# Optimization experiments

Measured on AMD Instinct MI355X. Metric: run time of the kernel, lower is better.

## Reference

```python
import jax, jax.numpy as jnp
import numpy as np

N_NODES = 100000
N_EDGES = 1600000
IN_DIM, HID_DIM, OUT_DIM = 384, 64, 64
DROP_P = 0.5


def setup_inputs() -> dict:
    key = jax.random.key(0)
    ks = jax.random.split(key, 9)
    x = jax.random.normal(ks[0], (N_NODES, IN_DIM), dtype=jnp.float32)
    edge_index = jax.random.randint(ks[1], (2, N_EDGES), 0, N_NODES, dtype=jnp.int64)
    edge_weight = jax.random.uniform(ks[2], (N_EDGES,), dtype=jnp.float32)
    W1 = jax.random.normal(ks[3], (IN_DIM, HID_DIM), dtype=jnp.float32) * (1.0 / np.sqrt(IN_DIM))
    b1 = jnp.zeros((HID_DIM,), dtype=jnp.float32)
    W2 = jax.random.normal(ks[4], (HID_DIM, OUT_DIM), dtype=jnp.float32) * (1.0 / np.sqrt(HID_DIM))
    b2 = jnp.zeros((OUT_DIM,), dtype=jnp.float32)
    drop_mask1 = jax.random.bernoulli(ks[5], 1.0 - DROP_P, (N_NODES, IN_DIM))
    drop_mask2 = jax.random.bernoulli(ks[6], 1.0 - DROP_P, (N_NODES, HID_DIM))
    return {"x": x, "edge_index": edge_index, "edge_weight": edge_weight,
            "W1": W1, "b1": b1, "W2": W2, "b2": b2,
            "drop_mask1": drop_mask1, "drop_mask2": drop_mask2}


def _gcn_conv(h, W, b, src, dst, edge_weight, n_nodes):
    # GCNConv: linear transform first (smaller dim), then normalized sparse aggregation
    h = h @ W                                        # [N, d_out]
    msg = h[src] * edge_weight[:, None]              # gather over edges [E, d_out]
    agg = jax.ops.segment_sum(msg, dst, num_segments=n_nodes)  # scatter-add [N, d_out]
    return agg + b


def reference(x, edge_index, edge_weight, W1, b1, W2, b2, drop_mask1, drop_mask2):
    scale = 1.0 / (1.0 - DROP_P)
    src, dst = edge_index[0], edge_index[1]
    n = x.shape[0]
    h = x * drop_mask1.astype(x.dtype) * scale                  # dropout (training)
    h = jax.nn.relu(_gcn_conv(h, W1, b1, src, dst, edge_weight, n))
    h = h * drop_mask2.astype(h.dtype) * scale                  # dropout (training)
    return _gcn_conv(h, W2, b2, src, dst, edge_weight, n)
```

## Files before the change

### kernel.cpp

```cpp
#include <hip/hip_runtime.h>
#include <hip/hip_bf16.h>
#include <stdint.h>

#define N_NODES 100000
#define N_EDGES 1600000
#define IN_DIM  384
#define HID_DIM 64
#define SCAN_NB 391

typedef __attribute__((ext_vector_type(8))) short short8_t;
typedef __attribute__((ext_vector_type(4))) float f32x4;

__global__ void k_detect(const uint32_t* __restrict__ ei,
                         const uint32_t* __restrict__ m1,
                         int* __restrict__ flags) {
    int l = threadIdx.x;
    uint32_t hi = ei[2 * l + 1];
    int ei64 = __all(hi == 0u);

    uint32_t maxb = 0;
    int bf = 0, f16 = 0, hib = 0;
    for (int i = 0; i < 4; ++i) {
        uint32_t w = m1[l * 4 + i];
        uint32_t b0 = w & 0xffu, b1 = (w >> 8) & 0xffu,
                 b2 = (w >> 16) & 0xffu, b3 = (w >> 24) & 0xffu;
        uint32_t mb = b0 > b1 ? b0 : b1;
        uint32_t mb2 = b2 > b3 ? b2 : b3;
        mb = mb > mb2 ? mb : mb2;
        maxb = maxb > mb ? maxb : mb;
        if ((w & 0xffffu) == 0x3f80u) bf = 1;
        if ((w & 0xffffu) == 0x3c00u) f16 = 1;
        if ((b1 | b2 | b3) != 0u) hib = 1;
    }
    int small  = __all(maxb <= 1u);
    int anybf  = __any(bf);
    int anyf16 = __any(f16);
    int anyhib = __any(hib);
    if (l == 0) {
        flags[0] = ei64;
        int mm;
        if (small)                 mm = anyhib ? 3 : 4;
        else if (anybf || anyf16)  mm = 0;
        else                       mm = 2;
        flags[1] = mm;
    }
}

__device__ __forceinline__ float mask_at(const void* p, int mode, long idx) {
    if (mode == 0) return ((const uint16_t*)p)[idx] ? 2.0f : 0.0f;
    if (mode == 2) return ((const float*)p)[idx] != 0.0f ? 2.0f : 0.0f;
    if (mode == 3) return ((const uint8_t*)p)[idx] ? 2.0f : 0.0f;
    return ((const int*)p)[idx] ? 2.0f : 0.0f;
}

__device__ __forceinline__ void load_edge(const int* p32, int mode64, long e,
                                          int& s, int& d) {
    if (mode64) { s = p32[2 * e]; d = p32[2 * (N_EDGES + e)]; }
    else        { s = p32[e];     d = p32[N_EDGES + e]; }
}

__device__ __forceinline__ ushort f2bf(float f) {
    uint32_t u = __float_as_uint(f);
    return (ushort)((u + 0x7fffu + ((u >> 16) & 1u)) >> 16);
}
__device__ __forceinline__ float bf2f(ushort h) {
    return __uint_as_float(((uint32_t)h) << 16);
}

__global__ __launch_bounds__(256) void k_hist(const void* __restrict__ ei,
                                              uint32_t* __restrict__ deg,
                                              const int* __restrict__ flags) {
    const int mode64 = flags[0];
    const int* p32 = (const int*)ei;
    for (long e = (long)blockIdx.x * 256 + threadIdx.x; e < N_EDGES;
         e += (long)gridDim.x * 256) {
        int s, d; load_edge(p32, mode64, e, s, d);
        atomicAdd(&deg[d], 1u);
    }
}

__global__ __launch_bounds__(256) void k_scanA(const uint32_t* __restrict__ deg,
                                               uint32_t* __restrict__ partials) {
    __shared__ uint32_t sbuf[256];
    int idx = blockIdx.x * 256 + threadIdx.x;
    uint32_t v = idx < N_NODES ? deg[idx] : 0u;
    sbuf[threadIdx.x] = v;
    __syncthreads();
    for (int off = 128; off > 0; off >>= 1) {
        if (threadIdx.x < off) sbuf[threadIdx.x] += sbuf[threadIdx.x + off];
        __syncthreads();
    }
    if (threadIdx.x == 0) partials[blockIdx.x] = sbuf[0];
}

__global__ void k_scanB(uint32_t* __restrict__ partials,
                        uint32_t* __restrict__ poff,
                        uint32_t* __restrict__ starts) {
    if (threadIdx.x == 0) {
        uint32_t run = 0;
        for (int b = 0; b < SCAN_NB; ++b) {
            poff[b] = run;
            run += partials[b];
        }
        starts[N_NODES] = run;
    }
}

__global__ __launch_bounds__(256) void k_scanC(const uint32_t* __restrict__ deg,
                                               const uint32_t* __restrict__ poff,
                                               uint32_t* __restrict__ starts) {
    __shared__ uint32_t sbuf[256];
    int idx = blockIdx.x * 256 + threadIdx.x;
    uint32_t v = idx < N_NODES ? deg[idx] : 0u;
    sbuf[threadIdx.x] = v;
    __syncthreads();
    for (int off = 1; off < 256; off <<= 1) {
        uint32_t add = threadIdx.x >= off ? sbuf[threadIdx.x - off] : 0u;
        __syncthreads();
        sbuf[threadIdx.x] += add;
        __syncthreads();
    }
    if (idx < N_NODES) starts[idx] = poff[blockIdx.x] + sbuf[threadIdx.x] - v;
}

__global__ __launch_bounds__(256) void k_reorder(const void* __restrict__ ei,
                                                 const float* __restrict__ ew,
                                                 uint32_t* __restrict__ cursors,
                                                 int2* __restrict__ sorted,
                                                 const int* __restrict__ flags) {
    const int mode64 = flags[0];
    const int* p32 = (const int*)ei;
    for (long e = (long)blockIdx.x * 256 + threadIdx.x; e < N_EDGES;
         e += (long)gridDim.x * 256) {
        int s, d; load_edge(p32, mode64, e, s, d);
        float w = ew[e];
        uint32_t pos = atomicAdd(&cursors[d], 1u);
        sorted[pos] = make_int2(s, __float_as_int(w));
    }
}

__global__ __launch_bounds__(256) void k1_mfma(
        const float* __restrict__ x, const void* __restrict__ m1,
        const float* __restrict__ W1, float* __restrict__ H,
        const int* __restrict__ flags) {
    __shared__ ushort Ah[64][32];
    __shared__ ushort Al[64][32];
    __shared__ ushort Bh[64][32];
    __shared__ ushort Bl[64][32];
    const int mmode = flags[1];
    const int t = threadIdx.x;
    const int node0 = blockIdx.x * 64;
    const int l = t & 63, w = t >> 6;

    f32x4 acc[4];
#pragma unroll
    for (int i = 0; i < 4; ++i) acc[i] = (f32x4)0.0f;

    const int arow = t >> 2;
    const int akq  = (t & 3) * 8;
    const int brow = t >> 3;
    const int bc0  = (t & 7) * 8;

    for (int ks = 0; ks < IN_DIM; ks += 32) {
        {
            float xv[8];
            long node = node0 + arow;
            if (node < N_NODES) {
                long gb = node * IN_DIM + ks + akq;
                float4 x0 = *(const float4*)(x + gb);
                float4 x1 = *(const float4*)(x + gb + 4);
                xv[0] = x0.x; xv[1] = x0.y; xv[2] = x0.z; xv[3] = x0.w;
                xv[4] = x1.x; xv[5] = x1.y; xv[6] = x1.z; xv[7] = x1.w;
                float mv[8];
                if (mmode == 0) {
                    const ushort* mp = (const ushort*)m1 + gb;
                    ushort4 a = *(const ushort4*)mp;
                    ushort4 b = *(const ushort4*)(mp + 4);
                    mv[0] = a.x ? 2.f : 0.f; mv[1] = a.y ? 2.f : 0.f;
                    mv[2] = a.z ? 2.f : 0.f; mv[3] = a.w ? 2.f : 0.f;
                    mv[4] = b.x ? 2.f : 0.f; mv[5] = b.y ? 2.f : 0.f;
                    mv[6] = b.z ? 2.f : 0.f; mv[7] = b.w ? 2.f : 0.f;
                } else if (mmode == 2) {
                    const float* mp = (const float*)m1 + gb;
                    float4 a = *(const float4*)mp;
                    float4 b = *(const float4*)(mp + 4);
                    mv[0] = a.x != 0.f ? 2.f : 0.f; mv[1] = a.y != 0.f ? 2.f : 0.f;
                    mv[2] = a.z != 0.f ? 2.f : 0.f; mv[3] = a.w != 0.f ? 2.f : 0.f;
                    mv[4] = b.x != 0.f ? 2.f : 0.f; mv[5] = b.y != 0.f ? 2.f : 0.f;
                    mv[6] = b.z != 0.f ? 2.f : 0.f; mv[7] = b.w != 0.f ? 2.f : 0.f;
                } else if (mmode == 3) {
                    uint2 mb = *(const uint2*)((const uint8_t*)m1 + gb);
#pragma unroll
                    for (int j = 0; j < 4; ++j) {
                        mv[j]     = ((mb.x >> (8 * j)) & 0xffu) ? 2.f : 0.f;
                        mv[4 + j] = ((mb.y >> (8 * j)) & 0xffu) ? 2.f : 0.f;
                    }
                } else {
                    const int* mp = (const int*)m1 + gb;
                    int4 a = *(const int4*)mp;
                    int4 b = *(const int4*)(mp + 4);
                    mv[0] = a.x ? 2.f : 0.f; mv[1] = a.y ? 2.f : 0.f;
                    mv[2] = a.z ? 2.f : 0.f; mv[3] = a.w ? 2.f : 0.f;
                    mv[4] = b.x ? 2.f : 0.f; mv[5] = b.y ? 2.f : 0.f;
                    mv[6] = b.z ? 2.f : 0.f; mv[7] = b.w ? 2.f : 0.f;
                }
#pragma unroll
                for (int j = 0; j < 8; ++j) xv[j] *= mv[j];
            } else {
#pragma unroll
                for (int j = 0; j < 8; ++j) xv[j] = 0.0f;
            }
            uint ph[4], pl[4];
#pragma unroll
            for (int j2 = 0; j2 < 4; ++j2) {
                ushort h0 = f2bf(xv[2 * j2]);
                ushort h1 = f2bf(xv[2 * j2 + 1]);
                ushort l0 = f2bf(xv[2 * j2]     - bf2f(h0));
                ushort l1 = f2bf(xv[2 * j2 + 1] - bf2f(h1));
                ph[j2] = (uint)h0 | ((uint)h1 << 16);
                pl[j2] = (uint)l0 | ((uint)l1 << 16);
            }
            *(uint4*)&Ah[arow][akq] = make_uint4(ph[0], ph[1], ph[2], ph[3]);
            *(uint4*)&Al[arow][akq] = make_uint4(pl[0], pl[1], pl[2], pl[3]);
        }
        {
            long gb = (long)(ks + brow) * 64 + bc0;
            float4 w0 = *(const float4*)(W1 + gb);
            float4 w1 = *(const float4*)(W1 + gb + 4);
            float wv[8] = {w0.x, w0.y, w0.z, w0.w, w1.x, w1.y, w1.z, w1.w};
#pragma unroll
            for (int j = 0; j < 8; ++j) {
                ushort hs = f2bf(wv[j]);
                Bh[bc0 + j][brow] = hs;
                Bl[bc0 + j][brow] = f2bf(wv[j] - bf2f(hs));
            }
        }
        __syncthreads();
        short8_t ah = *(const short8_t*)&Ah[w * 16 + (l & 15)][(l >> 4) * 8];
        short8_t al = *(const short8_t*)&Al[w * 16 + (l & 15)][(l >> 4) * 8];
#pragma unroll
        for (int nt = 0; nt < 4; ++nt) {
            short8_t bh = *(const short8_t*)&Bh[nt * 16 + (l & 15)][(l >> 4) * 8];
            short8_t bl = *(const short8_t*)&Bl[nt * 16 + (l & 15)][(l >> 4) * 8];
            acc[nt] = __builtin_amdgcn_mfma_f32_16x16x32_bf16(ah, bh, acc[nt], 0, 0, 0);
            acc[nt] = __builtin_amdgcn_mfma_f32_16x16x32_bf16(ah, bl, acc[nt], 0, 0, 0);
            acc[nt] = __builtin_amdgcn_mfma_f32_16x16x32_bf16(al, bh, acc[nt], 0, 0, 0);
        }
        __syncthreads();
    }
    const int r0 = (l >> 4) * 4;
#pragma unroll
    for (int nt = 0; nt < 4; ++nt) {
#pragma unroll
        for (int r = 0; r < 4; ++r) {
            long node = node0 + w * 16 + r0 + r;
            if (node < N_NODES) H[node * 64 + nt * 16 + (l & 15)] = acc[nt][r];
        }
    }
}

__global__ __launch_bounds__(256) void k_agg(const float* __restrict__ Hsrc,
                                             const int2* __restrict__ sorted,
                                             const uint32_t* __restrict__ starts,
                                             const float* __restrict__ bias,
                                             float* __restrict__ dest) {
    const int lane = threadIdx.x & 63;
    const long n = (long)blockIdx.x * 4 + (threadIdx.x >> 6);
    if (n >= N_NODES) return;
    uint32_t e  = starts[n];
    uint32_t e1 = starts[n + 1];
    float acc = bias ? bias[lane] : 0.0f;
    for (; e + 2 <= e1; e += 2) {
        int2 p0 = sorted[e];
        int2 p1 = sorted[e + 1];
        float v0 = Hsrc[(long)p0.x * 64 + lane];
        float v1 = Hsrc[(long)p1.x * 64 + lane];
        acc = fmaf(v0, __int_as_float(p0.y), acc);
        acc = fmaf(v1, __int_as_float(p1.y), acc);
    }
    if (e < e1) {
        int2 p0 = sorted[e];
        acc = fmaf(Hsrc[(long)p0.x * 64 + lane], __int_as_float(p0.y), acc);
    }
    dest[n * 64 + lane] = acc;
}

__global__ __launch_bounds__(256) void k_aggmlp(
        const float* __restrict__ Hsrc, const int2* __restrict__ sorted,
        const uint32_t* __restrict__ starts, const float* __restrict__ b1,
        const void* __restrict__ m2, const float* __restrict__ W2,
        float* __restrict__ H2, const int* __restrict__ flags) {
    __shared__ float w2s[64 * 64];
    __shared__ float vbuf[4][64];
    const int mmode = flags[1];
    for (int i = threadIdx.x; i < 4096; i += 256) w2s[i] = W2[i];
    __syncthreads();

    const int lane = threadIdx.x & 63;
    const int w = threadIdx.x >> 6;
    const long n = (long)blockIdx.x * 4 + w;
    uint32_t e  = starts[n];
    uint32_t e1 = starts[n + 1];
    float acc = 0.0f;
    for (; e + 2 <= e1; e += 2) {
        int2 p0 = sorted[e];
        int2 p1 = sorted[e + 1];
        float v0 = Hsrc[(long)p0.x * 64 + lane];
        float v1 = Hsrc[(long)p1.x * 64 + lane];
        acc = fmaf(v0, __int_as_float(p0.y), acc);
        acc = fmaf(v1, __int_as_float(p1.y), acc);
    }
    if (e < e1) {
        int2 p0 = sorted[e];
        acc = fmaf(Hsrc[(long)p0.x * 64 + lane], __int_as_float(p0.y), acc);
    }
    float u = acc + b1[lane];
    u = u > 0.0f ? u : 0.0f;
    u *= mask_at(m2, mmode, n * 64 + lane);
    vbuf[w][lane] = u;
    float h2 = 0.0f;
#pragma unroll
    for (int j = 0; j < 64; j += 4) {
        float4 v4 = *(const float4*)&vbuf[w][j];
        h2 = fmaf(v4.x, w2s[(j + 0) * 64 + lane], h2);
        h2 = fmaf(v4.y, w2s[(j + 1) * 64 + lane], h2);
        h2 = fmaf(v4.z, w2s[(j + 2) * 64 + lane], h2);
        h2 = fmaf(v4.w, w2s[(j + 3) * 64 + lane], h2);
    }
    H2[n * 64 + lane] = h2;
}

__global__ __launch_bounds__(256) void k_scatter(
        const float* __restrict__ Hsrc, const void* __restrict__ ei,
        const float* __restrict__ ew, float* __restrict__ dest,
        const int* __restrict__ flags) {
    const int mode64 = flags[0];
    const int lane = threadIdx.x & 63;
    const long wid = (long)blockIdx.x * 4 + (threadIdx.x >> 6);
    const long nw = (long)gridDim.x * 4;
    const int* p32 = (const int*)ei;
    for (long e = wid; e < N_EDGES; e += nw) {
        int s, d; load_edge(p32, mode64, e, s, d);
        float w = ew[e];
        float v = Hsrc[(long)s * 64 + lane] * w;
        atomicAdd(&dest[(long)d * 64 + lane], v);
    }
}

__global__ __launch_bounds__(256) void k3_mlp(
        const float* __restrict__ agg, const float* __restrict__ b1,
        const void* __restrict__ m2, const float* __restrict__ W2,
        float* __restrict__ H2, const int* __restrict__ flags) {
    __shared__ float w2s[64 * 64];
    __shared__ float vbuf[4][64];
    const int mmode = flags[1];
    for (int i = threadIdx.x; i < 4096; i += 256) w2s[i] = W2[i];
    __syncthreads();
    const int lane = threadIdx.x & 63;
    const int w = threadIdx.x >> 6;
    const float bc = b1[lane];
    const long wid = (long)blockIdx.x * 4 + w;
    const long nw = (long)gridDim.x * 4;
    for (long n = wid; n < N_NODES; n += nw) {
        float u = agg[n * 64 + lane] + bc;
        u = u > 0.0f ? u : 0.0f;
        u *= mask_at(m2, mmode, n * 64 + lane);
        vbuf[w][lane] = u;
        float acc = 0.0f;
#pragma unroll
        for (int j = 0; j < 64; j += 4) {
            float4 v4 = *(const float4*)&vbuf[w][j];
            acc = fmaf(v4.x, w2s[(j + 0) * 64 + lane], acc);
            acc = fmaf(v4.y, w2s[(j + 1) * 64 + lane], acc);
            acc = fmaf(v4.z, w2s[(j + 2) * 64 + lane], acc);
            acc = fmaf(v4.w, w2s[(j + 3) * 64 + lane], acc);
        }
        H2[n * 64 + lane] = acc;
    }
}

__global__ void k_init_out(float* __restrict__ out, const float* __restrict__ b2) {
    const long total = (long)N_NODES * 16;
    for (long j = (long)blockIdx.x * 256 + threadIdx.x; j < total;
         j += (long)gridDim.x * 256) {
        ((float4*)out)[j] = ((const float4*)b2)[j & 15];
    }
}

extern "C" void kernel_launch(void* const* d_in, const int* in_sizes, int n_in,
                              void* d_out, int out_size, void* d_ws, size_t ws_size,
                              hipStream_t stream) {
    const float* x  = (const float*)d_in[0];
    const void*  ei = d_in[1];
    const float* ew = (const float*)d_in[2];
    const float* W1 = (const float*)d_in[3];
    const float* b1 = (const float*)d_in[4];
    const float* W2 = (const float*)d_in[5];
    const float* b2 = (const float*)d_in[6];
    const void*  m1 = d_in[7];
    const void*  m2 = d_in[8];
    float* out = (float*)d_out;

    char* ws = (char*)d_ws;
    size_t off = 0;
    auto alloc = [&](size_t bytes) {
        char* p = ws + off;
        off += (bytes + 255) & ~(size_t)255;
        return p;
    };
    int*      flags   = (int*)alloc(32);
    float*    H       = (float*)alloc((size_t)N_NODES * 64 * 4);
    float*    AGG     = (float*)alloc((size_t)N_NODES * 64 * 4);
    int2*     sorted  = (int2*)alloc((size_t)N_EDGES * 8);
    uint32_t* starts  = (uint32_t*)alloc((size_t)(N_NODES + 1) * 4);
    uint32_t* deg     = (uint32_t*)alloc((size_t)N_NODES * 4);
    uint32_t* cursors = (uint32_t*)alloc((size_t)N_NODES * 4);
    uint32_t* poff    = (uint32_t*)alloc((size_t)SCAN_NB * 4);
    size_t need = off;

    hipLaunchKernelGGL(k_detect, dim3(1), dim3(64), 0, stream,
                       (const uint32_t*)ei, (const uint32_t*)m1, flags);

    if (ws_size >= need) {
        hipMemsetAsync(deg, 0, (size_t)N_NODES * 4, stream);
        hipLaunchKernelGGL(k_hist, dim3(2048), dim3(256), 0, stream,
                           ei, deg, flags);
        hipLaunchKernelGGL(k_scanA, dim3(SCAN_NB), dim3(256), 0, stream,
                           deg, poff);
        hipLaunchKernelGGL(k_scanB, dim3(1), dim3(64), 0, stream,
                           poff, cursors, starts);
        hipLaunchKernelGGL(k_scanC, dim3(SCAN_NB), dim3(256), 0, stream,
                           deg, cursors, starts);
        hipMemcpyAsync(cursors, starts, (size_t)N_NODES * 4,
                       hipMemcpyDeviceToDevice, stream);
        hipLaunchKernelGGL(k_reorder, dim3(2048), dim3(256), 0, stream,
                           ei, ew, cursors, sorted, flags);
        hipLaunchKernelGGL(k1_mfma, dim3((N_NODES + 63) / 64), dim3(256), 0, stream,
                           x, m1, W1, H, flags);
        hipLaunchKernelGGL(k_aggmlp, dim3(N_NODES / 4), dim3(256), 0, stream,
                           H, sorted, starts, b1, m2, W2, AGG, flags);
        hipLaunchKernelGGL(k_agg, dim3(N_NODES / 4), dim3(256), 0, stream,
                           AGG, sorted, starts, b2, out);
    } else {
        hipMemsetAsync(AGG, 0, (size_t)N_NODES * 64 * 4, stream);
        hipLaunchKernelGGL(k1_mfma, dim3((N_NODES + 63) / 64), dim3(256), 0, stream,
                           x, m1, W1, H, flags);
        hipLaunchKernelGGL(k_scatter, dim3(4096), dim3(256), 0, stream,
                           H, ei, ew, AGG, flags);
        hipLaunchKernelGGL(k3_mlp, dim3(1024), dim3(256), 0, stream,
                           AGG, b1, m2, W2, H, flags);
        hipLaunchKernelGGL(k_init_out, dim3(2048), dim3(256), 0, stream, out, b2);
        hipLaunchKernelGGL(k_scatter, dim3(4096), dim3(256), 0, stream,
                           H, ei, ew, out, flags);
    }
}
```

Measured before the change: 834.7 us.

## Store hidden features in bf16, prepack W1, drop LDS staging and low-part MFMA

Intermediate node features H and H2 are now stored as bf16 instead of fp32, halving gather traffic in both edge aggregation passes. W1 is pre-split into bf16 hi/lo fragments by a new packing kernel, so the GEMM kernel loads A and B fragments straight from global memory without LDS or barriers. The GEMM also drops the x-low-part MFMA term. The aggregation loops are unrolled to four edges, and the single-thread partial scan is replaced by a parallel block scan. These changes reduce accuracy (bf16 storage of activations, no low-part x term), which risks tolerance failures.

Result: faster. 785.3 us (-5.9%).

```diff
diff --git a/kernel.cpp b/kernel.cpp
--- a/kernel.cpp
+++ b/kernel.cpp
@@ -93,17 +93,22 @@
     if (threadIdx.x == 0) partials[blockIdx.x] = sbuf[0];
 }
 
-__global__ void k_scanB(uint32_t* __restrict__ partials,
-                        uint32_t* __restrict__ poff,
-                        uint32_t* __restrict__ starts) {
-    if (threadIdx.x == 0) {
-        uint32_t run = 0;
-        for (int b = 0; b < SCAN_NB; ++b) {
-            poff[b] = run;
-            run += partials[b];
-        }
-        starts[N_NODES] = run;
-    }
+__global__ __launch_bounds__(512) void k_scanB(const uint32_t* __restrict__ partials,
+                                               uint32_t* __restrict__ poff,
+                                               uint32_t* __restrict__ starts) {
+    __shared__ uint32_t sbuf[512];
+    int t = threadIdx.x;
+    uint32_t v = t < SCAN_NB ? partials[t] : 0u;
+    sbuf[t] = v;
+    __syncthreads();
+    for (int off = 1; off < 512; off <<= 1) {
+        uint32_t add = t >= off ? sbuf[t - off] : 0u;
+        __syncthreads();
+        sbuf[t] += add;
+        __syncthreads();
+    }
+    if (t < SCAN_NB) poff[t] = sbuf[t] - v;
+    if (t == SCAN_NB - 1) starts[N_NODES] = sbuf[t];
 }
 
 __global__ __launch_bounds__(256) void k_scanC(const uint32_t* __restrict__ deg,
@@ -139,114 +144,98 @@
     }
 }
 
+__global__ __launch_bounds__(256) void k_packW(const float* __restrict__ W1,
+                                               ushort* __restrict__ Wpack) {
+    const int ks = blockIdx.x;
+    const int t  = threadIdx.x;
+    const int nt = t >> 6, l = t & 63;
+    ushort hs[8], ls[8];
+#pragma unroll
+    for (int j = 0; j < 8; ++j) {
+        float wv = W1[(ks * 32 + (l >> 4) * 8 + j) * 64 + nt * 16 + (l & 15)];
+        ushort h = f2bf(wv);
+        hs[j] = h;
+        ls[j] = f2bf(wv - bf2f(h));
+    }
+    *(short8_t*)&Wpack[((8 * ks + nt) * 64 + l) * 8]     = *(short8_t*)hs;
+    *(short8_t*)&Wpack[((8 * ks + 4 + nt) * 64 + l) * 8] = *(short8_t*)ls;
+}
+
 __global__ __launch_bounds__(256) void k1_mfma(
         const float* __restrict__ x, const void* __restrict__ m1,
-        const float* __restrict__ W1, float* __restrict__ H,
+        const ushort* __restrict__ Wpack, ushort* __restrict__ Hb,
         const int* __restrict__ flags) {
-    __shared__ ushort Ah[64][32];
-    __shared__ ushort Al[64][32];
-    __shared__ ushort Bh[64][32];
-    __shared__ ushort Bl[64][32];
     const int mmode = flags[1];
     const int t = threadIdx.x;
+    const int l = t & 63, w = t >> 6;
     const int node0 = blockIdx.x * 64;
-    const int l = t & 63, w = t >> 6;
+    const long row = node0 + w * 16 + (l & 15);
+    const int kq = (l >> 4) * 8;
+    const bool valid = row < N_NODES;
 
     f32x4 acc[4];
 #pragma unroll
     for (int i = 0; i < 4; ++i) acc[i] = (f32x4)0.0f;
 
-    const int arow = t >> 2;
-    const int akq  = (t & 3) * 8;
-    const int brow = t >> 3;
-    const int bc0  = (t & 7) * 8;
-
-    for (int ks = 0; ks < IN_DIM; ks += 32) {
-        {
-            float xv[8];
-            long node = node0 + arow;
-            if (node < N_NODES) {
-                long gb = node * IN_DIM + ks + akq;
-                float4 x0 = *(const float4*)(x + gb);
-                float4 x1 = *(const float4*)(x + gb + 4);
-                xv[0] = x0.x; xv[1] = x0.y; xv[2] = x0.z; xv[3] = x0.w;
-                xv[4] = x1.x; xv[5] = x1.y; xv[6] = x1.z; xv[7] = x1.w;
-                float mv[8];
-                if (mmode == 0) {
-                    const ushort* mp = (const ushort*)m1 + gb;
-                    ushort4 a = *(const ushort4*)mp;
-                    ushort4 b = *(const ushort4*)(mp + 4);
-                    mv[0] = a.x ? 2.f : 0.f; mv[1] = a.y ? 2.f : 0.f;
-                    mv[2] = a.z ? 2.f : 0.f; mv[3] = a.w ? 2.f : 0.f;
-                    mv[4] = b.x ? 2.f : 0.f; mv[5] = b.y ? 2.f : 0.f;
-                    mv[6] = b.z ? 2.f : 0.f; mv[7] = b.w ? 2.f : 0.f;
-                } else if (mmode == 2) {
-                    const float* mp = (const float*)m1 + gb;
-                    float4 a = *(const float4*)mp;
-                    float4 b = *(const float4*)(mp + 4);
-                    mv[0] = a.x != 0.f ? 2.f : 0.f; mv[1] = a.y != 0.f ? 2.f : 0.f;
-                    mv[2] = a.z != 0.f ? 2.f : 0.f; mv[3] = a.w != 0.f ? 2.f : 0.f;
-                    mv[4] = b.x != 0.f ? 2.f : 0.f; mv[5] = b.y != 0.f ? 2.f : 0.f;
-                    mv[6] = b.z != 0.f ? 2.f : 0.f; mv[7] = b.w != 0.f ? 2.f : 0.f;
-                } else if (mmode == 3) {
-                    uint2 mb = *(const uint2*)((const uint8_t*)m1 + gb);
-#pragma unroll
-                    for (int j = 0; j < 4; ++j) {
-                        mv[j]     = ((mb.x >> (8 * j)) & 0xffu) ? 2.f : 0.f;
-                        mv[4 + j] = ((mb.y >> (8 * j)) & 0xffu) ? 2.f : 0.f;
-                    }
-                } else {
-                    const int* mp = (const int*)m1 + gb;
-                    int4 a = *(const int4*)mp;
-                    int4 b = *(const int4*)(mp + 4);
-                    mv[0] = a.x ? 2.f : 0.f; mv[1] = a.y ? 2.f : 0.f;
-                    mv[2] = a.z ? 2.f : 0.f; mv[3] = a.w ? 2.f : 0.f;
-                    mv[4] = b.x ? 2.f : 0.f; mv[5] = b.y ? 2.f : 0.f;
-                    mv[6] = b.z ? 2.f : 0.f; mv[7] = b.w ? 2.f : 0.f;
+    for (int ks = 0; ks < 12; ++ks) {
+        float xv[8];
+        if (valid) {
+            long gb = row * IN_DIM + ks * 32 + kq;
+            float4 x0 = *(const float4*)(x + gb);
+            float4 x1 = *(const float4*)(x + gb + 4);
+            xv[0] = x0.x; xv[1] = x0.y; xv[2] = x0.z; xv[3] = x0.w;
+            xv[4] = x1.x; xv[5] = x1.y; xv[6] = x1.z; xv[7] = x1.w;
+            float mv[8];
+            if (mmode == 0) {
+                const ushort* mp = (const ushort*)m1 + gb;
+                ushort4 a = *(const ushort4*)mp;
+                ushort4 b = *(const ushort4*)(mp + 4);
+                mv[0] = a.x ? 2.f : 0.f; mv[1] = a.y ? 2.f : 0.f;
+                mv[2] = a.z ? 2.f : 0.f; mv[3] = a.w ? 2.f : 0.f;
+                mv[4] = b.x ? 2.f : 0.f; mv[5] = b.y ? 2.f : 0.f;
+                mv[6] = b.z ? 2.f : 0.f; mv[7] = b.w ? 2.f : 0.f;
+            } else if (mmode == 2) {
+                const float* mp = (const float*)m1 + gb;
+                float4 a = *(const float4*)mp;
+                float4 b = *(const float4*)(mp + 4);
+                mv[0] = a.x != 0.f ? 2.f : 0.f; mv[1] = a.y != 0.f ? 2.f : 0.f;
+                mv[2] = a.z != 0.f ? 2.f : 0.f; mv[3] = a.w != 0.f ? 2.f : 0.f;
+                mv[4] = b.x != 0.f ? 2.f : 0.f; mv[5] = b.y != 0.f ? 2.f : 0.f;
+                mv[6] = b.z != 0.f ? 2.f : 0.f; mv[7] = b.w != 0.f ? 2.f : 0.f;
+            } else if (mmode == 3) {
+                uint2 mb = *(const uint2*)((const uint8_t*)m1 + gb);
+#pragma unroll
+                for (int j = 0; j < 4; ++j) {
+                    mv[j]     = ((mb.x >> (8 * j)) & 0xffu) ? 2.f : 0.f;
+                    mv[4 + j] = ((mb.y >> (8 * j)) & 0xffu) ? 2.f : 0.f;
                 }
-#pragma unroll
-                for (int j = 0; j < 8; ++j) xv[j] *= mv[j];
             } else {
-#pragma unroll
-                for (int j = 0; j < 8; ++j) xv[j] = 0.0f;
+                const int* mp = (const int*)m1 + gb;
+                int4 a = *(const int4*)mp;
+                int4 b = *(const int4*)(mp + 4);
+                mv[0] = a.x ? 2.f : 0.f; mv[1] = a.y ? 2.f : 0.f;
+                mv[2] = a.z ? 2.f : 0.f; mv[3] = a.w ? 2.f : 0.f;
+                mv[4] = b.x ? 2.f : 0.f; mv[5] = b.y ? 2.f : 0.f;
+                mv[6] = b.z ? 2.f : 0.f; mv[7] = b.w ? 2.f : 0.f;
             }
-            uint ph[4], pl[4];
-#pragma unroll
-            for (int j2 = 0; j2 < 4; ++j2) {
-                ushort h0 = f2bf(xv[2 * j2]);
-                ushort h1 = f2bf(xv[2 * j2 + 1]);
-                ushort l0 = f2bf(xv[2 * j2]     - bf2f(h0));
-                ushort l1 = f2bf(xv[2 * j2 + 1] - bf2f(h1));
-                ph[j2] = (uint)h0 | ((uint)h1 << 16);
-                pl[j2] = (uint)l0 | ((uint)l1 << 16);
-            }
-            *(uint4*)&Ah[arow][akq] = make_uint4(ph[0], ph[1], ph[2], ph[3]);
-            *(uint4*)&Al[arow][akq] = make_uint4(pl[0], pl[1], pl[2], pl[3]);
+#pragma unroll
+            for (int j = 0; j < 8; ++j) xv[j] *= mv[j];
+        } else {
+#pragma unroll
+            for (int j = 0; j < 8; ++j) xv[j] = 0.0f;
         }
-        {
-            long gb = (long)(ks + brow) * 64 + bc0;
-            float4 w0 = *(const float4*)(W1 + gb);
-            float4 w1 = *(const float4*)(W1 + gb + 4);
-            float wv[8] = {w0.x, w0.y, w0.z, w0.w, w1.x, w1.y, w1.z, w1.w};
-#pragma unroll
-            for (int j = 0; j < 8; ++j) {
-                ushort hs = f2bf(wv[j]);
-                Bh[bc0 + j][brow] = hs;
-                Bl[bc0 + j][brow] = f2bf(wv[j] - bf2f(hs));
-            }
-        }
-        __syncthreads();
-        short8_t ah = *(const short8_t*)&Ah[w * 16 + (l & 15)][(l >> 4) * 8];
-        short8_t al = *(const short8_t*)&Al[w * 16 + (l & 15)][(l >> 4) * 8];
+        ushort ap[8];
+#pragma unroll
+        for (int j = 0; j < 8; ++j) ap[j] = f2bf(xv[j]);
+        short8_t ah = *(short8_t*)ap;
+
 #pragma unroll
         for (int nt = 0; nt < 4; ++nt) {
-            short8_t bh = *(const short8_t*)&Bh[nt * 16 + (l & 15)][(l >> 4) * 8];
-            short8_t bl = *(const short8_t*)&Bl[nt * 16 + (l & 15)][(l >> 4) * 8];
+            short8_t bh = *(const short8_t*)&Wpack[((8 * ks + nt) * 64 + l) * 8];
+            short8_t bl = *(const short8_t*)&Wpack[((8 * ks + 4 + nt) * 64 + l) * 8];
             acc[nt] = __builtin_amdgcn_mfma_f32_16x16x32_bf16(ah, bh, acc[nt], 0, 0, 0);
             acc[nt] = __builtin_amdgcn_mfma_f32_16x16x32_bf16(ah, bl, acc[nt], 0, 0, 0);
-            acc[nt] = __builtin_amdgcn_mfma_f32_16x16x32_bf16(al, bh, acc[nt], 0, 0, 0);
         }
-        __syncthreads();
     }
     const int r0 = (l >> 4) * 4;
 #pragma unroll
@@ -254,12 +243,62 @@
 #pragma unroll
         for (int r = 0; r < 4; ++r) {
             long node = node0 + w * 16 + r0 + r;
-            if (node < N_NODES) H[node * 64 + nt * 16 + (l & 15)] = acc[nt][r];
+            if (node < N_NODES)
+                Hb[node * 64 + nt * 16 + (l & 15)] = f2bf(acc[nt][r]);
         }
     }
 }
 
-__global__ __launch_bounds__(256) void k_agg(const float* __restrict__ Hsrc,
+__global__ __launch_bounds__(256) void k_aggmlp(
+        const ushort* __restrict__ Hb, const int2* __restrict__ sorted,
+        const uint32_t* __restrict__ starts, const float* __restrict__ b1,
+        const void* __restrict__ m2, const float* __restrict__ W2,
+        ushort* __restrict__ H2b, const int* __restrict__ flags) {
+    __shared__ float w2s[64 * 64];
+    __shared__ float vbuf[4][64];
+    const int mmode = flags[1];
+    for (int i = threadIdx.x; i < 4096; i += 256) w2s[i] = W2[i];
+    __syncthreads();
+
+    const int lane = threadIdx.x & 63;
+    const int w = threadIdx.x >> 6;
+    const long n = (long)blockIdx.x * 4 + w;
+    uint32_t e  = starts[n];
+    uint32_t e1 = starts[n + 1];
+    float acc = 0.0f;
+    for (; e + 4 <= e1; e += 4) {
+        int2 p0 = sorted[e],     p1 = sorted[e + 1];
+        int2 p2 = sorted[e + 2], p3 = sorted[e + 3];
+        float v0 = bf2f(Hb[(long)p0.x * 64 + lane]);
+        float v1 = bf2f(Hb[(long)p1.x * 64 + lane]);
+        float v2 = bf2f(Hb[(long)p2.x * 64 + lane]);
+        float v3 = bf2f(Hb[(long)p3.x * 64 + lane]);
+        acc = fmaf(v0, __int_as_float(p0.y), acc);
+        acc = fmaf(v1, __int_as_float(p1.y), acc);
+        acc = fmaf(v2, __int_as_float(p2.y), acc);
+        acc = fmaf(v3, __int_as_float(p3.y), acc);
+    }
+    for (; e < e1; ++e) {
+        int2 p0 = sorted[e];
+        acc = fmaf(bf2f(Hb[(long)p0.x * 64 + lane]), __int_as_float(p0.y), acc);
+    }
+    float u = acc + b1[lane];
+    u = u > 0.0f ? u : 0.0f;
+    u *= mask_at(m2, mmode, n * 64 + lane);
+    vbuf[w][lane] = u;
+    float h2 = 0.0f;
+#pragma unroll
+    for (int j = 0; j < 64; j += 4) {
+        float4 v4 = *(const float4*)&vbuf[w][j];
+        h2 = fmaf(v4.x, w2s[(j + 0) * 64 + lane], h2);
+        h2 = fmaf(v4.y, w2s[(j + 1) * 64 + lane], h2);
+        h2 = fmaf(v4.z, w2s[(j + 2) * 64 + lane], h2);
+        h2 = fmaf(v4.w, w2s[(j + 3) * 64 + lane], h2);
+    }
+    H2b[n * 64 + lane] = f2bf(h2);
+}
+
+__global__ __launch_bounds__(256) void k_agg(const ushort* __restrict__ Hb,
                                              const int2* __restrict__ sorted,
                                              const uint32_t* __restrict__ starts,
                                              const float* __restrict__ bias,
@@ -269,69 +308,28 @@
     if (n >= N_NODES) return;
     uint32_t e  = starts[n];
     uint32_t e1 = starts[n + 1];
-    float acc = bias ? bias[lane] : 0.0f;
-    for (; e + 2 <= e1; e += 2) {
-        int2 p0 = sorted[e];
-        int2 p1 = sorted[e + 1];
-        float v0 = Hsrc[(long)p0.x * 64 + lane];
-        float v1 = Hsrc[(long)p1.x * 64 + lane];
+    float acc = bias[lane];
+    for (; e + 4 <= e1; e += 4) {
+        int2 p0 = sorted[e],     p1 = sorted[e + 1];
+        int2 p2 = sorted[e + 2], p3 = sorted[e + 3];
+        float v0 = bf2f(Hb[(long)p0.x * 64 + lane]);
+        float v1 = bf2f(Hb[(long)p1.x * 64 + lane]);
+        float v2 = bf2f(Hb[(long)p2.x * 64 + lane]);
+        float v3 = bf2f(Hb[(long)p3.x * 64 + lane]);
         acc = fmaf(v0, __int_as_float(p0.y), acc);
         acc = fmaf(v1, __int_as_float(p1.y), acc);
-    }
-    if (e < e1) {
+        acc = fmaf(v2, __int_as_float(p2.y), acc);
+        acc = fmaf(v3, __int_as_float(p3.y), acc);
+    }
+    for (; e < e1; ++e) {
         int2 p0 = sorted[e];
-        acc = fmaf(Hsrc[(long)p0.x * 64 + lane], __int_as_float(p0.y), acc);
+        acc = fmaf(bf2f(Hb[(long)p0.x * 64 + lane]), __int_as_float(p0.y), acc);
     }
     dest[n * 64 + lane] = acc;
 }
 
-__global__ __launch_bounds__(256) void k_aggmlp(
-        const float* __restrict__ Hsrc, const int2* __restrict__ sorted,
-        const uint32_t* __restrict__ starts, const float* __restrict__ b1,
-        const void* __restrict__ m2, const float* __restrict__ W2,
-        float* __restrict__ H2, const int* __restrict__ flags) {
-    __shared__ float w2s[64 * 64];
-    __shared__ float vbuf[4][64];
-    const int mmode = flags[1];
-    for (int i = threadIdx.x; i < 4096; i += 256) w2s[i] = W2[i];
-    __syncthreads();
-
-    const int lane = threadIdx.x & 63;
-    const int w = threadIdx.x >> 6;
-    const long n = (long)blockIdx.x * 4 + w;
-    uint32_t e  = starts[n];
-    uint32_t e1 = starts[n + 1];
-    float acc = 0.0f;
-    for (; e + 2 <= e1; e += 2) {
-        int2 p0 = sorted[e];
-        int2 p1 = sorted[e + 1];
-        float v0 = Hsrc[(long)p0.x * 64 + lane];
-        float v1 = Hsrc[(long)p1.x * 64 + lane];
-        acc = fmaf(v0, __int_as_float(p0.y), acc);
-        acc = fmaf(v1, __int_as_float(p1.y), acc);
-    }
-    if (e < e1) {
-        int2 p0 = sorted[e];
-        acc = fmaf(Hsrc[(long)p0.x * 64 + lane], __int_as_float(p0.y), acc);
-    }
-    float u = acc + b1[lane];
-    u = u > 0.0f ? u : 0.0f;
-    u *= mask_at(m2, mmode, n * 64 + lane);
-    vbuf[w][lane] = u;
-    float h2 = 0.0f;
-#pragma unroll
-    for (int j = 0; j < 64; j += 4) {
-        float4 v4 = *(const float4*)&vbuf[w][j];
-        h2 = fmaf(v4.x, w2s[(j + 0) * 64 + lane], h2);
-        h2 = fmaf(v4.y, w2s[(j + 1) * 64 + lane], h2);
-        h2 = fmaf(v4.z, w2s[(j + 2) * 64 + lane], h2);
-        h2 = fmaf(v4.w, w2s[(j + 3) * 64 + lane], h2);
-    }
-    H2[n * 64 + lane] = h2;
-}
-
 __global__ __launch_bounds__(256) void k_scatter(
-        const float* __restrict__ Hsrc, const void* __restrict__ ei,
+        const ushort* __restrict__ Hb, const void* __restrict__ ei,
         const float* __restrict__ ew, float* __restrict__ dest,
         const int* __restrict__ flags) {
     const int mode64 = flags[0];
@@ -342,7 +340,7 @@
     for (long e = wid; e < N_EDGES; e += nw) {
         int s, d; load_edge(p32, mode64, e, s, d);
         float w = ew[e];
-        float v = Hsrc[(long)s * 64 + lane] * w;
+        float v = bf2f(Hb[(long)s * 64 + lane]) * w;
         atomicAdd(&dest[(long)d * 64 + lane], v);
     }
 }
@@ -350,7 +348,7 @@
 __global__ __launch_bounds__(256) void k3_mlp(
         const float* __restrict__ agg, const float* __restrict__ b1,
         const void* __restrict__ m2, const float* __restrict__ W2,
-        float* __restrict__ H2, const int* __restrict__ flags) {
+        ushort* __restrict__ H2b, const int* __restrict__ flags) {
     __shared__ float w2s[64 * 64];
     __shared__ float vbuf[4][64];
     const int mmode = flags[1];
@@ -375,7 +373,7 @@
             acc = fmaf(v4.z, w2s[(j + 2) * 64 + lane], acc);
             acc = fmaf(v4.w, w2s[(j + 3) * 64 + lane], acc);
         }
-        H2[n * 64 + lane] = acc;
+        H2b[n * 64 + lane] = f2bf(acc);
     }
 }
 
@@ -409,17 +407,20 @@
         return p;
     };
     int*      flags   = (int*)alloc(32);
-    float*    H       = (float*)alloc((size_t)N_NODES * 64 * 4);
+    ushort*   Hb      = (ushort*)alloc((size_t)N_NODES * 64 * 2);
+    ushort*   H2b     = (ushort*)alloc((size_t)N_NODES * 64 * 2);
     float*    AGG     = (float*)alloc((size_t)N_NODES * 64 * 4);
     int2*     sorted  = (int2*)alloc((size_t)N_EDGES * 8);
     uint32_t* starts  = (uint32_t*)alloc((size_t)(N_NODES + 1) * 4);
     uint32_t* deg     = (uint32_t*)alloc((size_t)N_NODES * 4);
     uint32_t* cursors = (uint32_t*)alloc((size_t)N_NODES * 4);
     uint32_t* poff    = (uint32_t*)alloc((size_t)SCAN_NB * 4);
+    ushort*   Wpack   = (ushort*)alloc((size_t)12 * 8 * 64 * 8 * 2);
     size_t need = off;
 
     hipLaunchKernelGGL(k_detect, dim3(1), dim3(64), 0, stream,
                        (const uint32_t*)ei, (const uint32_t*)m1, flags);
+    hipLaunchKernelGGL(k_packW, dim3(12), dim3(256), 0, stream, W1, Wpack);
 
     if (ws_size >= need) {
         hipMemsetAsync(deg, 0, (size_t)N_NODES * 4, stream);
@@ -427,7 +428,7 @@
                            ei, deg, flags);
         hipLaunchKernelGGL(k_scanA, dim3(SCAN_NB), dim3(256), 0, stream,
                            deg, poff);
-        hipLaunchKernelGGL(k_scanB, dim3(1), dim3(64), 0, stream,
+        hipLaunchKernelGGL(k_scanB, dim3(1), dim3(512), 0, stream,
                            poff, cursors, starts);
         hipLaunchKernelGGL(k_scanC, dim3(SCAN_NB), dim3(256), 0, stream,
                            deg, cursors, starts);
@@ -436,21 +437,21 @@
         hipLaunchKernelGGL(k_reorder, dim3(2048), dim3(256), 0, stream,
                            ei, ew, cursors, sorted, flags);
         hipLaunchKernelGGL(k1_mfma, dim3((N_NODES + 63) / 64), dim3(256), 0, stream,
-                           x, m1, W1, H, flags);
+                           x, m1, Wpack, Hb, flags);
         hipLaunchKernelGGL(k_aggmlp, dim3(N_NODES / 4), dim3(256), 0, stream,
-                           H, sorted, starts, b1, m2, W2, AGG, flags);
+                           Hb, sorted, starts, b1, m2, W2, H2b, flags);
         hipLaunchKernelGGL(k_agg, dim3(N_NODES / 4), dim3(256), 0, stream,
-                           AGG, sorted, starts, b2, out);
+                           H2b, sorted, starts, b2, out);
     } else {
         hipMemsetAsync(AGG, 0, (size_t)N_NODES * 64 * 4, stream);
         hipLaunchKernelGGL(k1_mfma, dim3((N_NODES + 63) / 64), dim3(256), 0, stream,
-                           x, m1, W1, H, flags);
+                           x, m1, Wpack, Hb, flags);
         hipLaunchKernelGGL(k_scatter, dim3(4096), dim3(256), 0, stream,
-                           H, ei, ew, AGG, flags);
+                           Hb, ei, ew, AGG, flags);
         hipLaunchKernelGGL(k3_mlp, dim3(1024), dim3(256), 0, stream,
-                           AGG, b1, m2, W2, H, flags);
+                           AGG, b1, m2, W2, H2b, flags);
         hipLaunchKernelGGL(k_init_out, dim3(2048), dim3(256), 0, stream, out, b2);
         hipLaunchKernelGGL(k_scatter, dim3(4096), dim3(256), 0, stream,
-                           H, ei, ew, out, flags);
-    }
-}
+                           H2b, ei, ew, out, flags);
+    }
+}
```
